# Kernel tuning notes

Hardware: AMD Instinct MI355X
Metric: run time of the kernel (lower is better)

## Reference

```python
import jax, jax.numpy as jnp
import numpy as np

D_MODEL = 1024
NUM_HEADS = 16
HEAD_DIM = D_MODEL // NUM_HEADS


def setup_inputs() -> dict:
    key = jax.random.key(0)
    ks = jax.random.split(key, 10)
    B, SQ, SKV = 2, 2048, 2048
    s = 1.0 / np.sqrt(D_MODEL)
    inp = {
        "query": jax.random.normal(ks[0], (B, SQ, D_MODEL), jnp.float32),
        "key_value": jax.random.normal(ks[1], (B, SKV, D_MODEL), jnp.float32),
        "Wq": jax.random.normal(ks[2], (D_MODEL, D_MODEL), jnp.float32) * s,
        "bq": jnp.zeros((D_MODEL,), jnp.float32),
        "Wk": jax.random.normal(ks[3], (D_MODEL, D_MODEL), jnp.float32) * s,
        "bk": jnp.zeros((D_MODEL,), jnp.float32),
        "Wv": jax.random.normal(ks[4], (D_MODEL, D_MODEL), jnp.float32) * s,
        "bv": jnp.zeros((D_MODEL,), jnp.float32),
        "Wo": jax.random.normal(ks[5], (D_MODEL, D_MODEL), jnp.float32) * s,
        "bo": jnp.zeros((D_MODEL,), jnp.float32),
    }
    return inp


def reference(query, key_value, Wq, bq, Wk, bk, Wv, bv, Wo, bo):
    B, SQ, _ = query.shape
    SKV = key_value.shape[1]
    # projections (torch Linear: x @ W^T + b)
    Q = query @ Wq.T + bq
    K = key_value @ Wk.T + bk
    V = key_value @ Wv.T + bv
    # [B, H, S, Dh]
    Q = Q.reshape(B, SQ, NUM_HEADS, HEAD_DIM).transpose(0, 2, 1, 3)
    K = K.reshape(B, SKV, NUM_HEADS, HEAD_DIM).transpose(0, 2, 1, 3)
    V = V.reshape(B, SKV, NUM_HEADS, HEAD_DIM).transpose(0, 2, 1, 3)
    scores = jnp.einsum("bhqd,bhkd->bhqk", Q, K) / np.sqrt(HEAD_DIM)
    # causal mask: position q may attend to kv positions <= q
    causal = jnp.tril(jnp.ones((SQ, SKV), bool))  # True = keep
    scores = jnp.where(causal[None, None], scores, -jnp.inf)
    attn = jax.nn.softmax(scores, axis=-1)
    # dropout is identity in eval mode
    out = jnp.einsum("bhqk,bhkd->bhqd", attn, V)
    out = out.transpose(0, 2, 1, 3).reshape(B, SQ, D_MODEL)
    return out @ Wo.T + bo
```

## Files before the change

kernel.cpp:

```cpp
#include <hip/hip_runtime.h>
#include <hip/hip_bf16.h>
#include <cstdint>
#include <type_traits>

#define DM 1024
#define HEADS 16
#define DH 64
#define SEQ 2048
#define BATCH 2

typedef __attribute__((ext_vector_type(8))) short bf16x8;
typedef __attribute__((ext_vector_type(4))) float f32x4;
typedef __attribute__((ext_vector_type(16))) float f32x16;
typedef __attribute__((ext_vector_type(2))) unsigned int u32x2;
typedef __attribute__((ext_vector_type(4))) unsigned int u32x4;

#define SCALE2 0.18033688011112042f

#define GLOAD(dst, ptr) \
    asm volatile("global_load_dwordx4 %0, %1, off" : "=v"(dst) : "v"(ptr) : "memory")

static __device__ __forceinline__ unsigned short f2bf(float f) {
    unsigned u = __builtin_bit_cast(unsigned, f);
    u = u + 0x7fffu + ((u >> 16) & 1u);
    return (unsigned short)(u >> 16);
}
static __device__ __forceinline__ float bf2f(unsigned short us) {
    return __builtin_bit_cast(float, (unsigned)us << 16);
}

__global__ __launch_bounds__(256) void cast_all_k(
    const float* __restrict__ q, const float* __restrict__ kv,
    const float* __restrict__ wq, const float* __restrict__ wk,
    const float* __restrict__ wv, const float* __restrict__ wo,
    unsigned short* __restrict__ qb, unsigned short* __restrict__ kvb,
    unsigned short* __restrict__ wqb, unsigned short* __restrict__ wkb,
    unsigned short* __restrict__ wvb, unsigned short* __restrict__ wob)
{
    int blk = blockIdx.x;
    const float* s; unsigned short* d; int base;
    if (blk < 2048)      { s = q;  d = qb;  base = 0; }
    else if (blk < 4096) { s = kv; d = kvb; base = 2048; }
    else if (blk < 4608) { s = wq; d = wqb; base = 4096; }
    else if (blk < 5120) { s = wk; d = wkb; base = 4608; }
    else if (blk < 5632) { s = wv; d = wvb; base = 5120; }
    else                 { s = wo; d = wob; base = 5632; }
    int i = ((blk - base) * 256 + threadIdx.x) * 8;
    float4 a = *(const float4*)(s + i);
    float4 b2 = *(const float4*)(s + i + 4);
    ushort4 o0, o1;
    o0.x = f2bf(a.x);  o0.y = f2bf(a.y);  o0.z = f2bf(a.z);  o0.w = f2bf(a.w);
    o1.x = f2bf(b2.x); o1.y = f2bf(b2.y); o1.z = f2bf(b2.z); o1.w = f2bf(b2.w);
    *(ushort4*)(d + i) = o0;
    *(ushort4*)(d + i + 4) = o1;
}

__global__ __launch_bounds__(256) void proj_qkv(
    const unsigned short* __restrict__ qb,
    const unsigned short* __restrict__ kvb,
    const unsigned short* __restrict__ Wall,
    const float* __restrict__ bq, const float* __restrict__ bk, const float* __restrict__ bv,
    unsigned short* __restrict__ Qp, unsigned short* __restrict__ Kp,
    unsigned short* __restrict__ Vt)
{
    constexpr int BK = 64, K = 1024;
    __shared__ alignas(16) unsigned short As[64 * BK];
    __shared__ alignas(16) unsigned short Bs[128 * BK];

    const int t = threadIdx.x;
    const int lane = t & 63;
    const int w = t >> 6;
    const int wn = w * 32;
    const int lr = lane & 15, lg = lane >> 4;
    const int m0 = blockIdx.x * 64, n0 = blockIdx.y * 128;
    const int region = (blockIdx.y >= 8) + (blockIdx.y >= 16);
    const unsigned short* A = (region == 0) ? qb : kvb;

    f32x4 acc[4][2] = {};
    const int srow = t >> 3;
    const int schunk = t & 7;

    for (int kt = 0; kt < K; kt += BK) {
#pragma unroll
        for (int c = 0; c < 2; c++) {
            int row = srow + c * 32;
            int gc = schunk ^ (row & 7);
            __builtin_amdgcn_global_load_lds(
                (const __attribute__((address_space(1))) unsigned int*)(A + (size_t)(m0 + row) * K + kt + gc * 8),
                (__attribute__((address_space(3))) unsigned int*)(&As[row * BK + schunk * 8]), 16, 0, 0);
        }
#pragma unroll
        for (int c = 0; c < 4; c++) {
            int row = srow + c * 32;
            int gc = schunk ^ (row & 7);
            __builtin_amdgcn_global_load_lds(
                (const __attribute__((address_space(1))) unsigned int*)(Wall + (size_t)(n0 + row) * K + kt + gc * 8),
                (__attribute__((address_space(3))) unsigned int*)(&Bs[row * BK + schunk * 8]), 16, 0, 0);
        }
        __syncthreads();
#pragma unroll
        for (int kk = 0; kk < 2; kk++) {
            bf16x8 af[4], bfr[2];
#pragma unroll
            for (int i = 0; i < 4; i++)
                af[i] = *(const bf16x8*)(&As[(i * 16 + lr) * BK + (((kk * 4 + lg) ^ (lr & 7))) * 8]);
#pragma unroll
            for (int jj = 0; jj < 2; jj++)
                bfr[jj] = *(const bf16x8*)(&Bs[(wn + jj * 16 + lr) * BK + (((kk * 4 + lg) ^ (lr & 7))) * 8]);
#pragma unroll
            for (int i = 0; i < 4; i++)
#pragma unroll
                for (int jj = 0; jj < 2; jj++)
                    acc[i][jj] = __builtin_amdgcn_mfma_f32_16x16x32_bf16(af[i], bfr[jj], acc[i][jj], 0, 0, 0);
        }
        __syncthreads();
    }

    if (region == 0) {
#pragma unroll
        for (int i = 0; i < 4; i++) {
            int rbase = m0 + i * 16 + lg * 4;
#pragma unroll
            for (int jj = 0; jj < 2; jj++) {
                int col = n0 + wn + jj * 16 + lr;
                float bvv = bq[col];
#pragma unroll
                for (int r = 0; r < 4; r++)
                    Qp[(size_t)(rbase + r) * 1024 + col] = f2bf((acc[i][jj][r] + bvv) * SCALE2);
            }
        }
    } else if (region == 1) {
#pragma unroll
        for (int i = 0; i < 4; i++) {
            int rbase = m0 + i * 16 + lg * 4;
#pragma unroll
            for (int jj = 0; jj < 2; jj++) {
                int col = n0 - 1024 + wn + jj * 16 + lr;
                float bvv = bk[col];
#pragma unroll
                for (int r = 0; r < 4; r++)
                    Kp[(size_t)(rbase + r) * 1024 + col] = f2bf(acc[i][jj][r] + bvv);
            }
        }
    } else {
        int bidx = m0 >> 11;
#pragma unroll
        for (int i = 0; i < 4; i++) {
            int s0 = (m0 & 2047) + i * 16 + lg * 4;
#pragma unroll
            for (int jj = 0; jj < 2; jj++) {
                int nv = n0 - 2048 + wn + jj * 16 + lr;
                float bvv = bv[nv];
                int hh = nv >> 6, dd = nv & 63;
                ushort4 st;
                st.x = f2bf(acc[i][jj][0] + bvv);
                st.y = f2bf(acc[i][jj][1] + bvv);
                st.z = f2bf(acc[i][jj][2] + bvv);
                st.w = f2bf(acc[i][jj][3] + bvv);
                *(ushort4*)(Vt + ((size_t)((bidx * HEADS + hh) * DH + dd)) * SEQ + s0) = st;
            }
        }
    }
}

__global__ __launch_bounds__(256) void gemm_o(
    const unsigned short* __restrict__ A,
    const unsigned short* __restrict__ Bw,
    const float* __restrict__ bias,
    float* __restrict__ C,
    int M, int N, int K)
{
    constexpr int BK = 64;
    __shared__ alignas(16) unsigned short As[64 * BK];
    __shared__ alignas(16) unsigned short Bs[128 * BK];

    const int t = threadIdx.x;
    const int lane = t & 63;
    const int w = t >> 6;
    const int wn = w * 32;
    const int lr = lane & 15, lg = lane >> 4;
    const int m0 = blockIdx.x * 64, n0 = blockIdx.y * 128;

    f32x4 acc[4][2] = {};
    const int srow = t >> 3;
    const int schunk = t & 7;

    for (int kt = 0; kt < K; kt += BK) {
#pragma unroll
        for (int c = 0; c < 2; c++) {
            int row = srow + c * 32;
            int gc = schunk ^ (row & 7);
            __builtin_amdgcn_global_load_lds(
                (const __attribute__((address_space(1))) unsigned int*)(A + (size_t)(m0 + row) * K + kt + gc * 8),
                (__attribute__((address_space(3))) unsigned int*)(&As[row * BK + schunk * 8]), 16, 0, 0);
        }
#pragma unroll
        for (int c = 0; c < 4; c++) {
            int row = srow + c * 32;
            int gc = schunk ^ (row & 7);
            __builtin_amdgcn_global_load_lds(
                (const __attribute__((address_space(1))) unsigned int*)(Bw + (size_t)(n0 + row) * K + kt + gc * 8),
                (__attribute__((address_space(3))) unsigned int*)(&Bs[row * BK + schunk * 8]), 16, 0, 0);
        }
        __syncthreads();
#pragma unroll
        for (int kk = 0; kk < 2; kk++) {
            bf16x8 af[4], bfr[2];
#pragma unroll
            for (int i = 0; i < 4; i++)
                af[i] = *(const bf16x8*)(&As[(i * 16 + lr) * BK + (((kk * 4 + lg) ^ (lr & 7))) * 8]);
#pragma unroll
            for (int jj = 0; jj < 2; jj++)
                bfr[jj] = *(const bf16x8*)(&Bs[(wn + jj * 16 + lr) * BK + (((kk * 4 + lg) ^ (lr & 7))) * 8]);
#pragma unroll
            for (int i = 0; i < 4; i++)
#pragma unroll
                for (int jj = 0; jj < 2; jj++)
                    acc[i][jj] = __builtin_amdgcn_mfma_f32_16x16x32_bf16(af[i], bfr[jj], acc[i][jj], 0, 0, 0);
        }
        __syncthreads();
    }

#pragma unroll
    for (int i = 0; i < 4; i++) {
        int rbase = m0 + i * 16 + lg * 4;
#pragma unroll
        for (int jj = 0; jj < 2; jj++) {
            int col = n0 + wn + jj * 16 + lr;
            float bvv = bias[col];
#pragma unroll
            for (int r = 0; r < 4; r++)
                C[(size_t)(rbase + r) * 1024 + col] = acc[i][jj][r] + bvv;
        }
    }
}

__global__ __launch_bounds__(256, 2) void attn_k(
    const unsigned short* __restrict__ Qp,
    const unsigned short* __restrict__ Kp,
    const unsigned short* __restrict__ Vt,
    unsigned short* __restrict__ Ctx,
    unsigned short* __restrict__ pO,
    float2* __restrict__ pML)
{
    __shared__ alignas(16) unsigned char ldsb[2 * 16384];

    const int lane = threadIdx.x & 63;
    const int w = threadIdx.x >> 6;
    const int x = blockIdx.x;
    const int bh = x & 31;
    const int g = 39 - (x >> 5);
    int c, p, S;
    if (g < 4)       { c = g;                    p = 0;            S = 1; }
    else if (g < 12) { c = 4 + ((g - 4) >> 1);   p = (g - 4) & 1;  S = 2; }
    else if (g < 24) { c = 8 + (g - 12) / 3;     p = (g - 12) % 3; S = 3; }
    else             { c = 12 + ((g - 24) >> 2); p = (g - 24) & 3; S = 4; }
    const int nb = 2 * c + 2;
    const int len0 = (nb + S - 1) / S;
    const int start = p * len0;
    const int len = min(len0, nb - start);

    const int b = bh >> 4, h = bh & 15;
    const int q0 = c * 128;
    const int lq = lane & 31;
    const int hi = lane >> 5;
    const int qq = q0 + w * 32 + lq;
    const int my_nb = (q0 + 32 * w + 95) >> 6;
    const int qmin = q0 + 32 * w;
    constexpr float THR = 11.5f;

    bf16x8 Qf[4];
    {
        u32x4 qtmp[4];
        const unsigned short* qb = Qp + (size_t)(b * SEQ + qq) * DM + h * DH + hi * 8;
#pragma unroll
        for (int d = 0; d < 4; d++) GLOAD(qtmp[d], qb + d * 16);
        asm volatile("s_waitcnt vmcnt(0)" ::: "memory");
        __builtin_amdgcn_sched_barrier(0);
#pragma unroll
        for (int d = 0; d < 4; d++) Qf[d] = __builtin_bit_cast(bf16x8, qtmp[d]);
    }

    const int colx = (((lane & 7) ^ (lane >> 3)) << 4);
    const char* kg[2];
    const char* vg[2];
#pragma unroll
    for (int u = 0; u < 2; u++) {
        int s = 2 * w + u;
        int row = 8 * s + (lane >> 3);
        kg[u] = (const char*)Kp + (((size_t)(b * SEQ + row) * DM + h * DH) * 2) + colx;
        vg[u] = (const char*)Vt + ((((size_t)(b * HEADS + h) * DH + row) * SEQ) * 2) + colx;
    }
    const int kxor = (lq & 7) << 4;

    auto stage = [&](int buf, int t) {
        int kboff_k = t * (64 * DM * 2);
        int kboff_v = t * 128;
#pragma unroll
        for (int u = 0; u < 2; u++) {
            int s = 2 * w + u;
            __builtin_amdgcn_global_load_lds(
                (const __attribute__((address_space(1))) unsigned int*)(kg[u] + kboff_k),
                (__attribute__((address_space(3))) unsigned int*)(&ldsb[buf * 16384 + s * 1024 + lane * 16]), 16, 0, 0);
            __builtin_amdgcn_global_load_lds(
                (const __attribute__((address_space(1))) unsigned int*)(vg[u] + kboff_v),
                (__attribute__((address_space(3))) unsigned int*)(&ldsb[buf * 16384 + 8192 + s * 1024 + lane * 16]), 16, 0, 0);
        }
    };

    f32x16 o0 = {}, o1 = {};
    float m_run = -1e30f, l_run = 0.f;
    const int qmh0 = qq - 4 * hi;

    stage(0, start);

    for (int it = 0; it < len; it++) {
        const int t = start + it;
        const int cur = it & 1;
        if (it + 1 < len) {
            stage(cur ^ 1, t + 1);
            asm volatile("s_waitcnt vmcnt(4)" ::: "memory");
        } else {
            asm volatile("s_waitcnt vmcnt(0)" ::: "memory");
        }
        __builtin_amdgcn_sched_barrier(0);
        __builtin_amdgcn_s_barrier();

        if (t < my_nb) {
            const unsigned char* Kb = &ldsb[cur * 16384];
            const unsigned char* Vb = Kb + 8192;
            const int kb = t * 64;

            bf16x8 KA[4], KB[4], Vc[4][2];
#pragma unroll
            for (int d = 0; d < 4; d++) {
                int col = (d * 32 + hi * 16) ^ kxor;
                KA[d] = *(const bf16x8*)(Kb + lq * 128 + col);
                KB[d] = *(const bf16x8*)(Kb + (lq + 32) * 128 + col);
            }
#pragma unroll
            for (int s = 0; s < 4; s++)
#pragma unroll
                for (int dt = 0; dt < 2; dt++)
                    Vc[s][dt] = *(const bf16x8*)(Vb + (dt * 32 + lq) * 128 + ((s * 32 + hi * 16) ^ kxor));

            f32x16 sa0 = {}, sa1 = {};
            __builtin_amdgcn_s_setprio(1);
#pragma unroll
            for (int d = 0; d < 4; d++) {
                sa0 = __builtin_amdgcn_mfma_f32_32x32x16_bf16(KA[d], Qf[d], sa0, 0, 0, 0);
                sa1 = __builtin_amdgcn_mfma_f32_32x32x16_bf16(KB[d], Qf[d], sa1, 0, 0, 0);
            }
            __builtin_amdgcn_s_setprio(0);

            if (kb + 63 > qmin) {
                const int qmh = qmh0 - kb;
#pragma unroll
                for (int r = 0; r < 16; r++) {
                    int kvl = (r & 3) + 8 * (r >> 2);
                    sa0[r] = (kvl <= qmh) ? sa0[r] : -1e30f;
                    sa1[r] = (kvl + 32 <= qmh) ? sa1[r] : -1e30f;
                }
            }
            float mx[16];
#pragma unroll
            for (int r = 0; r < 16; r++) mx[r] = fmaxf(sa0[r], sa1[r]);
#pragma unroll
            for (int r = 0; r < 8; r++) mx[r] = fmaxf(mx[r], mx[r + 8]);
#pragma unroll
            for (int r = 0; r < 4; r++) mx[r] = fmaxf(mx[r], mx[r + 4]);
            mx[0] = fmaxf(mx[0], mx[2]);
            mx[1] = fmaxf(mx[1], mx[3]);
            float mloc = fmaxf(mx[0], mx[1]);
            mloc = fmaxf(mloc, __shfl_xor(mloc, 32));

            if (!__all(mloc - m_run <= THR)) {
                float m_new = fmaxf(m_run, mloc);
                float sf = __builtin_amdgcn_exp2f(m_run - m_new);
                l_run *= sf;
#pragma unroll
                for (int r = 0; r < 16; r++) { o0[r] *= sf; o1[r] *= sf; }
                m_run = m_new;
            }

            float p0v[16], p1v[16];
#pragma unroll
            for (int r = 0; r < 16; r++) {
                p0v[r] = __builtin_amdgcn_exp2f(sa0[r] - m_run);
                p1v[r] = __builtin_amdgcn_exp2f(sa1[r] - m_run);
            }
            float s4[8];
#pragma unroll
            for (int r = 0; r < 8; r++) s4[r] = (p0v[r] + p0v[r + 8]) + (p1v[r] + p1v[r + 8]);
#pragma unroll
            for (int r = 0; r < 4; r++) s4[r] += s4[r + 4];
            float ps = (s4[0] + s4[1]) + (s4[2] + s4[3]);
            ps += __shfl_xor(ps, 32);
            l_run += ps;

            unsigned c0[8], c1[8];
#pragma unroll
            for (int ii = 0; ii < 8; ii++) {
                unsigned pk;
                asm("v_cvt_pk_bf16_f32 %0, %1, %2" : "=v"(pk) : "v"(p0v[2 * ii]), "v"(p0v[2 * ii + 1]));
                c0[ii] = pk;
                asm("v_cvt_pk_bf16_f32 %0, %1, %2" : "=v"(pk) : "v"(p1v[2 * ii]), "v"(p1v[2 * ii + 1]));
                c1[ii] = pk;
            }
            bf16x8 Pb[4];
            {
                u32x2 r02 = __builtin_amdgcn_permlane32_swap(c0[0], c0[2], false, false);
                u32x2 r13 = __builtin_amdgcn_permlane32_swap(c0[1], c0[3], false, false);
                u32x2 r46 = __builtin_amdgcn_permlane32_swap(c0[4], c0[6], false, false);
                u32x2 r57 = __builtin_amdgcn_permlane32_swap(c0[5], c0[7], false, false);
                u32x4 w0 = {r02.x, r13.x, r02.y, r13.y};
                u32x4 w1 = {r46.x, r57.x, r46.y, r57.y};
                Pb[0] = __builtin_bit_cast(bf16x8, w0);
                Pb[1] = __builtin_bit_cast(bf16x8, w1);
            }
            {
                u32x2 r02 = __builtin_amdgcn_permlane32_swap(c1[0], c1[2], false, false);
                u32x2 r13 = __builtin_amdgcn_permlane32_swap(c1[1], c1[3], false, false);
                u32x2 r46 = __builtin_amdgcn_permlane32_swap(c1[4], c1[6], false, false);
                u32x2 r57 = __builtin_amdgcn_permlane32_swap(c1[5], c1[7], false, false);
                u32x4 w0 = {r02.x, r13.x, r02.y, r13.y};
                u32x4 w1 = {r46.x, r57.x, r46.y, r57.y};
                Pb[2] = __builtin_bit_cast(bf16x8, w0);
                Pb[3] = __builtin_bit_cast(bf16x8, w1);
            }

            __builtin_amdgcn_s_setprio(1);
#pragma unroll
            for (int s = 0; s < 4; s++) {
                o0 = __builtin_amdgcn_mfma_f32_32x32x16_bf16(Vc[s][0], Pb[s], o0, 0, 0, 0);
                o1 = __builtin_amdgcn_mfma_f32_32x32x16_bf16(Vc[s][1], Pb[s], o1, 0, 0, 0);
            }
            __builtin_amdgcn_s_setprio(0);
        }
        __builtin_amdgcn_s_barrier();
    }

    if (S == 1) {
        float inv = 1.0f / l_run;
        unsigned short* cb = Ctx + (size_t)(b * SEQ + qq) * DM + h * DH + hi * 4;
#pragma unroll
        for (int gg = 0; gg < 4; gg++) {
            ushort4 s0, s1;
            s0.x = f2bf(o0[4 * gg + 0] * inv); s0.y = f2bf(o0[4 * gg + 1] * inv);
            s0.z = f2bf(o0[4 * gg + 2] * inv); s0.w = f2bf(o0[4 * gg + 3] * inv);
            s1.x = f2bf(o1[4 * gg + 0] * inv); s1.y = f2bf(o1[4 * gg + 1] * inv);
            s1.z = f2bf(o1[4 * gg + 2] * inv); s1.w = f2bf(o1[4 * gg + 3] * inv);
            *(ushort4*)(cb + gg * 8) = s0;
            *(ushort4*)(cb + 32 + gg * 8) = s1;
        }
        return;
    }

    const int slot = g - 4;
    const int qrow = w * 32 + lq;
    unsigned short* pb = pO + ((size_t)(bh * 36 + slot) * 8192) + qrow * 64 + hi * 4;
#pragma unroll
    for (int gg = 0; gg < 4; gg++) {
        ushort4 s0, s1;
        s0.x = f2bf(o0[4 * gg + 0]); s0.y = f2bf(o0[4 * gg + 1]);
        s0.z = f2bf(o0[4 * gg + 2]); s0.w = f2bf(o0[4 * gg + 3]);
        s1.x = f2bf(o1[4 * gg + 0]); s1.y = f2bf(o1[4 * gg + 1]);
        s1.z = f2bf(o1[4 * gg + 2]); s1.w = f2bf(o1[4 * gg + 3]);
        *(ushort4*)(pb + gg * 8) = s0;
        *(ushort4*)(pb + 32 + gg * 8) = s1;
    }
    if (hi == 0)
        pML[(size_t)(bh * 36 + slot) * 128 + qrow] = make_float2(m_run, l_run);
}

__global__ __launch_bounds__(256) void combine_k(
    const unsigned short* __restrict__ pO,
    const float2* __restrict__ pML,
    unsigned short* __restrict__ Ctx)
{
    const int x = blockIdx.x;
    const int bh = x & 31;
    const int c = (x >> 5) + 4;
    const int S = (c >> 2) + 1;
    int slot0;
    if (c < 8)       slot0 = 2 * (c - 4);
    else if (c < 12) slot0 = 8 + 3 * (c - 8);
    else             slot0 = 20 + 4 * (c - 12);
    const int b = bh >> 4, h = bh & 15;

    const int q = threadIdx.x >> 1;
    const int d0 = (threadIdx.x & 1) * 32;

    float m[4], l[4], wgt[4];
    float M = -1e30f;
#pragma unroll
    for (int i = 0; i < 4; i++) {
        if (i < S) {
            float2 ml = pML[(size_t)(bh * 36 + slot0 + i) * 128 + q];
            m[i] = ml.x; l[i] = ml.y;
            M = fmaxf(M, m[i]);
        }
    }
    float L = 0.f;
#pragma unroll
    for (int i = 0; i < 4; i++) {
        if (i < S) {
            wgt[i] = __builtin_amdgcn_exp2f(m[i] - M);
            L += l[i] * wgt[i];
        }
    }
    float invL = 1.0f / L;
#pragma unroll
    for (int i = 0; i < 4; i++) if (i < S) wgt[i] *= invL;

    unsigned short* cb = Ctx + (size_t)(b * SEQ + c * 128 + q) * DM + h * DH + d0;
#pragma unroll
    for (int dd = 0; dd < 32; dd += 8) {
        float acc[8] = {};
#pragma unroll
        for (int i = 0; i < 4; i++) {
            if (i < S) {
                const unsigned short* pp = pO + ((size_t)(bh * 36 + slot0 + i) * 8192) + q * 64 + d0 + dd;
                bf16x8 v = *(const bf16x8*)pp;
#pragma unroll
                for (int e = 0; e < 8; e++)
                    acc[e] += wgt[i] * bf2f((unsigned short)v[e]);
            }
        }
        ushort4 s0, s1;
        s0.x = f2bf(acc[0]); s0.y = f2bf(acc[1]); s0.z = f2bf(acc[2]); s0.w = f2bf(acc[3]);
        s1.x = f2bf(acc[4]); s1.y = f2bf(acc[5]); s1.z = f2bf(acc[6]); s1.w = f2bf(acc[7]);
        *(ushort4*)(cb + dd) = s0;
        *(ushort4*)(cb + dd + 4) = s1;
    }
}

extern "C" void kernel_launch(void* const* d_in, const int* in_sizes, int n_in,
                              void* d_out, int out_size, void* d_ws, size_t ws_size,
                              hipStream_t stream)
{
    const float* query = (const float*)d_in[0];
    const float* keyv  = (const float*)d_in[1];
    const float* Wq = (const float*)d_in[2];
    const float* bq = (const float*)d_in[3];
    const float* Wk = (const float*)d_in[4];
    const float* bk = (const float*)d_in[5];
    const float* Wv = (const float*)d_in[6];
    const float* bv = (const float*)d_in[7];
    const float* Wo = (const float*)d_in[8];
    const float* bo = (const float*)d_in[9];
    float* out = (float*)d_out;

    const int M = BATCH * SEQ;
    char* ws = (char*)d_ws;
    size_t off = 0;
    auto alloc = [&](size_t elems) { unsigned short* p = (unsigned short*)(ws + off); off += elems * 2; return p; };
    unsigned short* qb  = alloc((size_t)M * DM);
    unsigned short* kvb = alloc((size_t)M * DM);
    unsigned short* wqb = alloc((size_t)DM * DM);
    unsigned short* wkb = alloc((size_t)DM * DM);
    unsigned short* wvb = alloc((size_t)DM * DM);
    unsigned short* wob = alloc((size_t)DM * DM);
    unsigned short* Qp  = alloc((size_t)M * DM);
    unsigned short* Kp  = alloc((size_t)M * DM);
    unsigned short* Vt  = alloc((size_t)M * DM);
    unsigned short* Ctx = alloc((size_t)M * DM);

    unsigned short* pO  = (unsigned short*)(ws + 0);
    float2*         pML = (float2*)(ws + 20971520);

    cast_all_k<<<6144, 256, 0, stream>>>(query, keyv, Wq, Wk, Wv, Wo,
                                         qb, kvb, wqb, wkb, wvb, wob);

    proj_qkv<<<dim3(M / 64, 24), 256, 0, stream>>>(qb, kvb, wqb, bq, bk, bv, Qp, Kp, Vt);

    attn_k<<<dim3(1280), 256, 0, stream>>>(Qp, Kp, Vt, Ctx, pO, pML);
    combine_k<<<dim3(384), 256, 0, stream>>>(pO, pML, Ctx);

    gemm_o<<<dim3(M / 64, 8), 256, 0, stream>>>(Ctx, wob, bo, out, M, DM, DM);
}
```

Baseline: 111.9 us.

## Double attention query tile to 256 rows with 8 waves per block

The attention kernel now uses 512-thread blocks covering 256 query rows instead of 128. Each wave stages one K and one V slice per tile rather than two, so every K/V tile loaded into LDS is shared by twice as many queries. The split-KV job schedule becomes a lookup table ordered longest-first, and the partial-output and combine layouts are resized to match. The trade-off is fewer, larger blocks (640 instead of 1280), which gives coarser load balance and higher register and LDS pressure per CU.

```diff
diff --git a/kernel.cpp b/kernel.cpp
--- a/kernel.cpp
+++ b/kernel.cpp
@@ -28,6 +28,10 @@
 static __device__ __forceinline__ float bf2f(unsigned short us) {
     return __builtin_bit_cast(float, (unsigned)us << 16);
 }
+
+__device__ const signed char JOB_C[20] = {7,7,7,7, 5,5,5, 3,3, 1, 6,6,6,6, 4,4, 4, 2,2, 0};
+__device__ const signed char JOB_P[20] = {0,1,2,3, 0,1,2, 0,1, 0, 0,1,2,3, 0,1, 2, 0,1, 0};
+__device__ const signed char SLOT0[8]  = {0,0, 0,2, 4,7, 10,14};
 
 __global__ __launch_bounds__(256) void cast_all_k(
     const float* __restrict__ q, const float* __restrict__ kv,
@@ -235,7 +239,7 @@
     }
 }
 
-__global__ __launch_bounds__(256, 2) void attn_k(
+__global__ __launch_bounds__(512, 2) void attn_k(
     const unsigned short* __restrict__ Qp,
     const unsigned short* __restrict__ Kp,
     const unsigned short* __restrict__ Vt,
@@ -249,19 +253,17 @@
     const int w = threadIdx.x >> 6;
     const int x = blockIdx.x;
     const int bh = x & 31;
-    const int g = 39 - (x >> 5);
-    int c, p, S;
-    if (g < 4)       { c = g;                    p = 0;            S = 1; }
-    else if (g < 12) { c = 4 + ((g - 4) >> 1);   p = (g - 4) & 1;  S = 2; }
-    else if (g < 24) { c = 8 + (g - 12) / 3;     p = (g - 12) % 3; S = 3; }
-    else             { c = 12 + ((g - 24) >> 2); p = (g - 24) & 3; S = 4; }
-    const int nb = 2 * c + 2;
+    const int g = x >> 5;
+    const int c = JOB_C[g];
+    const int p = JOB_P[g];
+    const int S = (c >> 1) + 1;
+    const int nb = 4 * (c + 1);
     const int len0 = (nb + S - 1) / S;
     const int start = p * len0;
     const int len = min(len0, nb - start);
 
     const int b = bh >> 4, h = bh & 15;
-    const int q0 = c * 128;
+    const int q0 = c * 256;
     const int lq = lane & 31;
     const int hi = lane >> 5;
     const int qq = q0 + w * 32 + lq;
@@ -272,9 +274,9 @@
     bf16x8 Qf[4];
     {
         u32x4 qtmp[4];
-        const unsigned short* qb = Qp + (size_t)(b * SEQ + qq) * DM + h * DH + hi * 8;
-#pragma unroll
-        for (int d = 0; d < 4; d++) GLOAD(qtmp[d], qb + d * 16);
+        const unsigned short* qbp = Qp + (size_t)(b * SEQ + qq) * DM + h * DH + hi * 8;
+#pragma unroll
+        for (int d = 0; d < 4; d++) GLOAD(qtmp[d], qbp + d * 16);
         asm volatile("s_waitcnt vmcnt(0)" ::: "memory");
         __builtin_amdgcn_sched_barrier(0);
 #pragma unroll
@@ -282,30 +284,17 @@
     }
 
     const int colx = (((lane & 7) ^ (lane >> 3)) << 4);
-    const char* kg[2];
-    const char* vg[2];
-#pragma unroll
-    for (int u = 0; u < 2; u++) {
-        int s = 2 * w + u;
-        int row = 8 * s + (lane >> 3);
-        kg[u] = (const char*)Kp + (((size_t)(b * SEQ + row) * DM + h * DH) * 2) + colx;
-        vg[u] = (const char*)Vt + ((((size_t)(b * HEADS + h) * DH + row) * SEQ) * 2) + colx;
-    }
+    const char* kg = (const char*)Kp + (((size_t)(b * SEQ + 8 * w + (lane >> 3)) * DM + h * DH) * 2) + colx;
+    const char* vg = (const char*)Vt + ((((size_t)(b * HEADS + h) * DH + 8 * w + (lane >> 3)) * SEQ) * 2) + colx;
     const int kxor = (lq & 7) << 4;
 
     auto stage = [&](int buf, int t) {
-        int kboff_k = t * (64 * DM * 2);
-        int kboff_v = t * 128;
-#pragma unroll
-        for (int u = 0; u < 2; u++) {
-            int s = 2 * w + u;
-            __builtin_amdgcn_global_load_lds(
-                (const __attribute__((address_space(1))) unsigned int*)(kg[u] + kboff_k),
-                (__attribute__((address_space(3))) unsigned int*)(&ldsb[buf * 16384 + s * 1024 + lane * 16]), 16, 0, 0);
-            __builtin_amdgcn_global_load_lds(
-                (const __attribute__((address_space(1))) unsigned int*)(vg[u] + kboff_v),
-                (__attribute__((address_space(3))) unsigned int*)(&ldsb[buf * 16384 + 8192 + s * 1024 + lane * 16]), 16, 0, 0);
-        }
+        __builtin_amdgcn_global_load_lds(
+            (const __attribute__((address_space(1))) unsigned int*)(kg + (size_t)t * (64 * DM * 2)),
+            (__attribute__((address_space(3))) unsigned int*)(&ldsb[buf * 16384 + w * 1024 + lane * 16]), 16, 0, 0);
+        __builtin_amdgcn_global_load_lds(
+            (const __attribute__((address_space(1))) unsigned int*)(vg + t * 128),
+            (__attribute__((address_space(3))) unsigned int*)(&ldsb[buf * 16384 + 8192 + w * 1024 + lane * 16]), 16, 0, 0);
     };
 
     f32x16 o0 = {}, o1 = {};
@@ -319,7 +308,7 @@
         const int cur = it & 1;
         if (it + 1 < len) {
             stage(cur ^ 1, t + 1);
-            asm volatile("s_waitcnt vmcnt(4)" ::: "memory");
+            asm volatile("s_waitcnt vmcnt(2)" ::: "memory");
         } else {
             asm volatile("s_waitcnt vmcnt(0)" ::: "memory");
         }
@@ -456,9 +445,9 @@
         return;
     }
 
-    const int slot = g - 4;
+    const int slot = SLOT0[c] + p;
     const int qrow = w * 32 + lq;
-    unsigned short* pb = pO + ((size_t)(bh * 36 + slot) * 8192) + qrow * 64 + hi * 4;
+    unsigned short* pb = pO + ((size_t)(bh * 18 + slot) * 16384) + qrow * 64 + hi * 4;
 #pragma unroll
     for (int gg = 0; gg < 4; gg++) {
         ushort4 s0, s1;
@@ -470,22 +459,19 @@
         *(ushort4*)(pb + 32 + gg * 8) = s1;
     }
     if (hi == 0)
-        pML[(size_t)(bh * 36 + slot) * 128 + qrow] = make_float2(m_run, l_run);
-}
-
-__global__ __launch_bounds__(256) void combine_k(
+        pML[(size_t)(bh * 18 + slot) * 256 + qrow] = make_float2(m_run, l_run);
+}
+
+__global__ __launch_bounds__(512) void combine_k(
     const unsigned short* __restrict__ pO,
     const float2* __restrict__ pML,
     unsigned short* __restrict__ Ctx)
 {
     const int x = blockIdx.x;
     const int bh = x & 31;
-    const int c = (x >> 5) + 4;
-    const int S = (c >> 2) + 1;
-    int slot0;
-    if (c < 8)       slot0 = 2 * (c - 4);
-    else if (c < 12) slot0 = 8 + 3 * (c - 8);
-    else             slot0 = 20 + 4 * (c - 12);
+    const int c = (x >> 5) + 2;
+    const int S = (c >> 1) + 1;
+    const int slot0 = SLOT0[c];
     const int b = bh >> 4, h = bh & 15;
 
     const int q = threadIdx.x >> 1;
@@ -496,7 +482,7 @@
 #pragma unroll
     for (int i = 0; i < 4; i++) {
         if (i < S) {
-            float2 ml = pML[(size_t)(bh * 36 + slot0 + i) * 128 + q];
+            float2 ml = pML[(size_t)(bh * 18 + slot0 + i) * 256 + q];
             m[i] = ml.x; l[i] = ml.y;
             M = fmaxf(M, m[i]);
         }
@@ -513,14 +499,14 @@
 #pragma unroll
     for (int i = 0; i < 4; i++) if (i < S) wgt[i] *= invL;
 
-    unsigned short* cb = Ctx + (size_t)(b * SEQ + c * 128 + q) * DM + h * DH + d0;
+    unsigned short* cb = Ctx + (size_t)(b * SEQ + c * 256 + q) * DM + h * DH + d0;
 #pragma unroll
     for (int dd = 0; dd < 32; dd += 8) {
         float acc[8] = {};
 #pragma unroll
         for (int i = 0; i < 4; i++) {
             if (i < S) {
-                const unsigned short* pp = pO + ((size_t)(bh * 36 + slot0 + i) * 8192) + q * 64 + d0 + dd;
+                const unsigned short* pp = pO + ((size_t)(bh * 18 + slot0 + i) * 16384) + q * 64 + d0 + dd;
                 bf16x8 v = *(const bf16x8*)pp;
 #pragma unroll
                 for (int e = 0; e < 8; e++)
@@ -574,8 +560,8 @@
 
     proj_qkv<<<dim3(M / 64, 24), 256, 0, stream>>>(qb, kvb, wqb, bq, bk, bv, Qp, Kp, Vt);
 
-    attn_k<<<dim3(1280), 256, 0, stream>>>(Qp, Kp, Vt, Ctx, pO, pML);
-    combine_k<<<dim3(384), 256, 0, stream>>>(pO, pML, Ctx);
+    attn_k<<<dim3(640), 512, 0, stream>>>(Qp, Kp, Vt, Ctx, pO, pML);
+    combine_k<<<dim3(192), 512, 0, stream>>>(pO, pML, Ctx);
 
     gemm_o<<<dim3(M / 64, 8), 256, 0, stream>>>(Ctx, wob, bo, out, M, DM, DM);
 }
```

Measured after the change: 120.8 us. +8.0%, slower.
